# Optimization experiments

Hardware: AMD Instinct MI355X
Metric: run time of the kernel (lower is better)

Reference implementation:

```python
import jax, jax.numpy as jnp
import numpy as np
from jax import lax

S, B, I, H, T = 512, 256, 227, 100, 19


def setup_inputs() -> dict:
    key = jax.random.key(0)
    ks = jax.random.split(key, 16)
    k = 1.0 / np.sqrt(H)
    u = lambda kk, shp: jax.random.uniform(kk, shp, jnp.float32, -k, k)
    return {
        "x": jax.random.normal(ks[0], (S, B, I), jnp.float32),
        "tags": jax.random.randint(ks[1], (S, B), 0, T),
        "w_ih_f": u(ks[2], (H, I)), "w_hh_f": u(ks[3], (H, H)),
        "b_ih_f": u(ks[4], (H,)), "b_hh_f": u(ks[5], (H,)),
        "w_ih_b": u(ks[6], (H, I)), "w_hh_b": u(ks[7], (H, H)),
        "b_ih_b": u(ks[8], (H,)), "b_hh_b": u(ks[9], (H,)),
        "W_tag": u(ks[10], (T, 2 * H)), "b_tag": u(ks[11], (T,)),
        "start_t": jax.random.uniform(ks[12], (T,), jnp.float32, -0.1, 0.1),
        "end_t": jax.random.uniform(ks[13], (T,), jnp.float32, -0.1, 0.1),
        "trans": jax.random.uniform(ks[14], (T, T), jnp.float32, -0.1, 0.1),
    }


def _rnn_dir(x_proj, w_hh, b_hh):
    # x_proj: (S, B, H) precomputed input projection; tanh Elman RNN scan
    def step(h, xt):
        h = jnp.tanh(xt + h @ w_hh.T + b_hh)
        return h, h
    h0 = jnp.zeros(x_proj.shape[1:3][:1] + (w_hh.shape[0],), x_proj.dtype)
    h0 = jnp.zeros((x_proj.shape[1], w_hh.shape[0]), x_proj.dtype)
    _, hs = lax.scan(step, h0, x_proj)
    return hs  # (S, B, H)


def reference(x, tags, w_ih_f, w_hh_f, b_ih_f, b_hh_f,
              w_ih_b, w_hh_b, b_ih_b, b_hh_b,
              W_tag, b_tag, start_t, end_t, trans):
    # Bidirectional RNN
    xf = jnp.einsum('sbi,hi->sbh', x, w_ih_f) + b_ih_f
    xb = jnp.einsum('sbi,hi->sbh', x, w_ih_b) + b_ih_b
    hf = _rnn_dir(xf, w_hh_f, b_hh_f)
    hb = _rnn_dir(xb[::-1], w_hh_b, b_hh_b)[::-1]
    h = jnp.concatenate([hf, hb], axis=-1)            # (S, B, 2H)
    emissions = jnp.einsum('sbh,th->sbt', h, W_tag) + b_tag  # (S, B, T)

    # CRF numerator: score of gold tag path
    em_score = jnp.take_along_axis(emissions, tags[:, :, None], axis=2)[:, :, 0].sum(0)
    tr_score = trans[tags[:-1], tags[1:]].sum(0)
    numerator = start_t[tags[0]] + em_score + tr_score + end_t[tags[-1]]  # (B,)

    # CRF partition function: forward algorithm (log-space DP over T=19 tags)
    def fstep(score, em_t):
        # score: (B, T) -> logsumexp over previous tag
        nxt = jax.nn.logsumexp(score[:, :, None] + trans[None] + em_t[:, None, :], axis=1)
        return nxt, None
    score0 = start_t[None, :] + emissions[0]
    score, _ = lax.scan(fstep, score0, emissions[1:])
    denominator = jax.nn.logsumexp(score + end_t[None, :], axis=1)  # (B,)

    # torchcrf default reduction='sum'
    return (numerator - denominator).sum()
```

## Files before the change

kernel.cpp:

```cpp
#include <hip/hip_runtime.h>
#include <hip/hip_bf16.h>
#include <math.h>

#define S_LEN 512
#define B_SZ  256
#define I_SZ  227
#define H_SZ  100
#define T_SZ  19

__device__ __forceinline__ float tanh_fast(float x) {
    float e = __expf(2.0f * x);
    return 1.0f - 2.0f / (e + 1.0f);
}

#define LXPAD 232
__global__ __launch_bounds__(256, 2)
void k1_inproj(const float* __restrict__ x,
               const float* __restrict__ w_ih_f, const float* __restrict__ b_ih_f,
               const float* __restrict__ w_ih_b, const float* __restrict__ b_ih_b,
               float* __restrict__ xf, float* __restrict__ xb) {
    __shared__ float lx[64 * LXPAD];
    const int tid  = threadIdx.x;
    const int lane = tid & 63;
    const long m0  = (long)blockIdx.x * 64;

    {
        const int cg = tid >> 6;
        const int c0 = cg * 57;
        const int nc = (cg == 3) ? 56 : 57;
        const float* src = x + (m0 + lane) * I_SZ;
        float* dst = lx + lane * LXPAD;
        for (int i = 0; i < nc; ++i) dst[c0 + i] = src[c0 + i];
    }
    __syncthreads();

    const int jb = __builtin_amdgcn_readfirstlane(tid >> 6) * 50;
    const float* xrow = lx + lane * LXPAD;

    float acc[5][10];
    #pragma unroll
    for (int g = 0; g < 5; ++g) {
        const int j0 = jb + g * 10;
        const float* wr[10];
        #pragma unroll
        for (int u = 0; u < 10; ++u) {
            int j = j0 + u;
            if (j < 100) { wr[u] = w_ih_f + (long)j * I_SZ;         acc[g][u] = b_ih_f[j]; }
            else         { wr[u] = w_ih_b + (long)(j - 100) * I_SZ; acc[g][u] = b_ih_b[j - 100]; }
        }
        for (int k = 0; k < 224; k += 4) {
            float4 xv = *(const float4*)(xrow + k);
            #pragma unroll
            for (int u = 0; u < 10; ++u) {
                acc[g][u] = fmaf(xv.x, wr[u][k],     acc[g][u]);
                acc[g][u] = fmaf(xv.y, wr[u][k + 1], acc[g][u]);
                acc[g][u] = fmaf(xv.z, wr[u][k + 2], acc[g][u]);
                acc[g][u] = fmaf(xv.w, wr[u][k + 3], acc[g][u]);
            }
        }
        #pragma unroll
        for (int k = 224; k < 227; ++k) {
            float xv = xrow[k];
            #pragma unroll
            for (int u = 0; u < 10; ++u) acc[g][u] = fmaf(xv, wr[u][k], acc[g][u]);
        }
    }

    __syncthreads();
    #pragma unroll
    for (int g = 0; g < 5; ++g) {
        #pragma unroll
        for (int u = 0; u < 10; ++u) {
            int j = jb + g * 10 + u;
            int base = (j < 100) ? (lane * 100 + j) : (6400 + lane * 100 + (j - 100));
            lx[base] = acc[g][u];
        }
    }
    __syncthreads();

    float* dstf = xf + m0 * 100;
    float* dstb = xb + m0 * 100;
    for (int i = tid; i < 1600; i += 256) {
        ((float4*)dstf)[i] = ((const float4*)lx)[i];
        ((float4*)dstb)[i] = ((const float4*)(lx + 6400))[i];
    }
}

#define HPAD 104
__global__ __launch_bounds__(128, 1)
void k2_rnn(const float* __restrict__ w_hh_f, const float* __restrict__ b_hh_f,
            const float* __restrict__ w_hh_b, const float* __restrict__ b_hh_b,
            float* __restrict__ xf, float* __restrict__ xb) {
    __shared__ float hbuf[2][HPAD];
    const int tid = threadIdx.x;
    const int j   = tid;
    const int b   = blockIdx.x & 255;
    const int dir = blockIdx.x >> 8;

    const float* whh = dir ? w_hh_b : w_hh_f;
    const float* bhh = dir ? b_hh_b : b_hh_f;
    float* xp        = dir ? xb : xf;

    float wreg[HPAD];
    #pragma unroll
    for (int k = 0; k < HPAD; ++k) wreg[k] = 0.f;
    float bias = 0.f;
    if (j < 100) {
        bias = bhh[j];
        #pragma unroll
        for (int k = 0; k < 100; ++k) wreg[k] = whh[j * 100 + k];
    }
    if (tid < HPAD) { hbuf[0][tid] = 0.f; hbuf[1][tid] = 0.f; }
    __syncthreads();

    const int jj = (j < 100) ? j : 0;
    float cur = xp[((long)(dir ? S_LEN - 1 : 0) * B_SZ + b) * 100 + jj];

    int p = 0;
    for (int t = 0; t < S_LEN; ++t) {
        const int s  = dir ? (S_LEN - 1 - t) : t;
        const int t2 = (t + 1 < S_LEN) ? (t + 1) : t;
        const int sn = dir ? (S_LEN - 1 - t2) : t2;
        float nxt = xp[((long)sn * B_SZ + b) * 100 + jj];

        float a0 = bias, a1 = 0.f, a2 = 0.f, a3 = 0.f;
        #pragma unroll
        for (int kk = 0; kk < 26; ++kk) {
            float4 hv = *(const float4*)&hbuf[p][kk * 4];
            a0 = fmaf(wreg[4 * kk],     hv.x, a0);
            a1 = fmaf(wreg[4 * kk + 1], hv.y, a1);
            a2 = fmaf(wreg[4 * kk + 2], hv.z, a2);
            a3 = fmaf(wreg[4 * kk + 3], hv.w, a3);
        }
        float hval = tanh_fast(cur + ((a0 + a1) + (a2 + a3)));
        if (j < 100) {
            xp[((long)s * B_SZ + b) * 100 + j] = hval;
            hbuf[p ^ 1][j] = hval;
        }
        __syncthreads();
        p ^= 1;
        cur = nxt;
    }
}

__global__ __launch_bounds__(256, 4)
void k4_emis(const float* __restrict__ hf, const float* __restrict__ hb,
             const float* __restrict__ W_tag, const float* __restrict__ b_tag,
             float* __restrict__ em) {
    __shared__ float lw[T_SZ * 200];
    __shared__ float lout[64 * T_SZ];
    const int tid = threadIdx.x;
    const long m0 = (long)blockIdx.x * 64;

    for (int i = tid; i < 950; i += 256)
        ((float4*)lw)[i] = ((const float4*)W_tag)[i];
    __syncthreads();

    const int r  = tid & 63;
    const int tg = __builtin_amdgcn_readfirstlane(tid >> 6);
    const float* hfr = hf + (m0 + r) * 100;
    const float* hbr = hb + (m0 + r) * 100;

    float acc[5];
    #pragma unroll
    for (int u = 0; u < 5; ++u) {
        int t = tg + 4 * u;
        acc[u] = (t < T_SZ) ? b_tag[t] : 0.f;
    }
    for (int k = 0; k < 100; k += 4) {
        float4 hv = *(const float4*)(hfr + k);
        float4 gv = *(const float4*)(hbr + k);
        #pragma unroll
        for (int u = 0; u < 5; ++u) {
            int t = tg + 4 * u;
            if (t < T_SZ) {
                float4 wv = *(const float4*)&lw[t * 200 + k];
                float4 vv = *(const float4*)&lw[t * 200 + 100 + k];
                acc[u] = fmaf(hv.x, wv.x, acc[u]); acc[u] = fmaf(hv.y, wv.y, acc[u]);
                acc[u] = fmaf(hv.z, wv.z, acc[u]); acc[u] = fmaf(hv.w, wv.w, acc[u]);
                acc[u] = fmaf(gv.x, vv.x, acc[u]); acc[u] = fmaf(gv.y, vv.y, acc[u]);
                acc[u] = fmaf(gv.z, vv.z, acc[u]); acc[u] = fmaf(gv.w, vv.w, acc[u]);
            }
        }
    }
    #pragma unroll
    for (int u = 0; u < 5; ++u) {
        int t = tg + 4 * u;
        if (t < T_SZ) lout[r * T_SZ + t] = acc[u];
    }
    __syncthreads();

    float* dst = em + m0 * T_SZ;
    for (int i = tid; i < 304; i += 256)
        ((float4*)dst)[i] = ((const float4*)lout)[i];
}

__global__ __launch_bounds__(64)
void k5_numer(const int* __restrict__ tags, const float* __restrict__ em,
              const float* __restrict__ trans, const float* __restrict__ start_t,
              const float* __restrict__ end_t, float* __restrict__ num) {
    const int b   = blockIdx.x;
    const int tid = threadIdx.x;
    float acc = 0.f;
    #pragma unroll
    for (int i = 0; i < 8; ++i) {
        int s  = tid + i * 64;
        int ts = tags[(long)s * B_SZ + b];
        acc += em[((long)s * B_SZ + b) * T_SZ + ts];
        if (s < S_LEN - 1) {
            int tn = tags[(long)(s + 1) * B_SZ + b];
            acc += trans[ts * T_SZ + tn];
        }
    }
    if (tid == 0)  acc += start_t[tags[b]];
    if (tid == 63) acc += end_t[tags[(long)(S_LEN - 1) * B_SZ + b]];
    #pragma unroll
    for (int off = 32; off; off >>= 1) acc += __shfl_down(acc, off, 64);
    if (tid == 0) num[b] = acc;
}

__global__ __launch_bounds__(64)
void k6_crf(const float* __restrict__ em, const float* __restrict__ trans,
            const float* __restrict__ start_t, const float* __restrict__ end_t,
            const float* __restrict__ num, float* __restrict__ out) {
    __shared__ float sbuf[2][3][20];
    const int tid = threadIdx.x;
    const int bl  = tid / T_SZ;
    const int j   = tid - bl * T_SZ;
    const int b   = blockIdx.x * 3 + bl;
    const bool act = (tid < 57) && (b < B_SZ);

    float texp[T_SZ];
    float score = 0.f, em_cur = 0.f;
    if (act) {
        #pragma unroll
        for (int i = 0; i < T_SZ; ++i) texp[i] = __expf(trans[i * T_SZ + j]);
        score  = start_t[j] + em[(long)b * T_SZ + j];
        em_cur = em[((long)1 * B_SZ + b) * T_SZ + j];
    }

    int buf = 0;
    for (int s = 1; s < S_LEN; ++s) {
        float em_nxt = 0.f;
        if (act) {
            int sn = (s + 1 < S_LEN) ? (s + 1) : s;
            em_nxt = em[((long)sn * B_SZ + b) * T_SZ + j];
            sbuf[buf][bl][j] = score;
        }
        __syncthreads();
        if (act) {
            float4 v0 = *(const float4*)&sbuf[buf][bl][0];
            float4 v1 = *(const float4*)&sbuf[buf][bl][4];
            float4 v2 = *(const float4*)&sbuf[buf][bl][8];
            float4 v3 = *(const float4*)&sbuf[buf][bl][12];
            float4 v4 = *(const float4*)&sbuf[buf][bl][16];
            float sc[T_SZ] = {v0.x,v0.y,v0.z,v0.w, v1.x,v1.y,v1.z,v1.w,
                              v2.x,v2.y,v2.z,v2.w, v3.x,v3.y,v3.z,v3.w,
                              v4.x,v4.y,v4.z};
            float m = sc[0];
            #pragma unroll
            for (int i = 0; i < 9; ++i) m = fmaxf(fmaxf(m, sc[2*i+1]), sc[2*i+2]);
            float sum = 0.f;
            #pragma unroll
            for (int i = 0; i < T_SZ; ++i) sum = fmaf(__expf(sc[i] - m), texp[i], sum);
            score = m + __logf(sum) + em_cur;
        }
        em_cur = em_nxt;
        buf ^= 1;
    }

    if (act) sbuf[0][bl][j] = score + end_t[j];
    __syncthreads();
    if (act && j == 0) {
        float m = -1e30f;
        #pragma unroll
        for (int i = 0; i < T_SZ; ++i) m = fmaxf(m, sbuf[0][bl][i]);
        float sum = 0.f;
        #pragma unroll
        for (int i = 0; i < T_SZ; ++i) sum += __expf(sbuf[0][bl][i] - m);
        atomicAdd(out, num[b] - (m + __logf(sum)));
    }
}

extern "C" void kernel_launch(void* const* d_in, const int* in_sizes, int n_in,
                              void* d_out, int out_size, void* d_ws, size_t ws_size,
                              hipStream_t stream) {
    const float* x       = (const float*)d_in[0];
    const int*   tags    = (const int*)  d_in[1];
    const float* w_ih_f  = (const float*)d_in[2];
    const float* w_hh_f  = (const float*)d_in[3];
    const float* b_ih_f  = (const float*)d_in[4];
    const float* b_hh_f  = (const float*)d_in[5];
    const float* w_ih_b  = (const float*)d_in[6];
    const float* w_hh_b  = (const float*)d_in[7];
    const float* b_ih_b  = (const float*)d_in[8];
    const float* b_hh_b  = (const float*)d_in[9];
    const float* W_tag   = (const float*)d_in[10];
    const float* b_tag   = (const float*)d_in[11];
    const float* start_t = (const float*)d_in[12];
    const float* end_t   = (const float*)d_in[13];
    const float* trans   = (const float*)d_in[14];

    float* ws = (float*)d_ws;
    float* xf  = ws;
    float* xb  = xf + 13107200;
    float* em  = xb + 13107200;
    float* num = em + 2490368;

    k1_inproj<<<2048, 256, 0, stream>>>(x, w_ih_f, b_ih_f, w_ih_b, b_ih_b, xf, xb);
    k2_rnn   <<<512, 128, 0, stream>>>(w_hh_f, b_hh_f, w_hh_b, b_hh_b, xf, xb);
    k4_emis  <<<2048, 256, 0, stream>>>(xf, xb, W_tag, b_tag, em);
    k5_numer <<<256, 64, 0, stream>>>(tags, em, trans, start_t, end_t, num);
    hipMemsetAsync(d_out, 0, sizeof(float), stream);
    k6_crf   <<<86, 64, 0, stream>>>(em, trans, start_t, end_t, num, (float*)d_out);
}
```

Before: 1.528 ms.

## Stage input-projection weights in LDS and coalesce x tile loads

The input-projection kernel now copies the 64-row x tile with coalesced float4 global loads, then remaps it into padded LDS rows. Each wave stages 25 weight rows at a time in its own LDS region and reads them as float4 from LDS, where before it read scalar weights from global memory. It keeps 50 accumulators per thread and uses dynamic shared memory of about 150 KB, with launch bounds lowered to one block per CU. The aim is to remove uncoalesced global weight reads and strided x loads, at the cost of lower occupancy, more LDS traffic and extra barriers.

```diff
diff --git a/kernel.cpp b/kernel.cpp
--- a/kernel.cpp
+++ b/kernel.cpp
@@ -13,68 +13,86 @@
     return 1.0f - 2.0f / (e + 1.0f);
 }
 
-#define LXPAD 232
-__global__ __launch_bounds__(256, 2)
+#define XTP 228
+#define K1_LDS ((64 + 4 * 25) * XTP * 4)
+
+__global__ __launch_bounds__(256, 1)
 void k1_inproj(const float* __restrict__ x,
                const float* __restrict__ w_ih_f, const float* __restrict__ b_ih_f,
                const float* __restrict__ w_ih_b, const float* __restrict__ b_ih_b,
                float* __restrict__ xf, float* __restrict__ xb) {
-    __shared__ float lx[64 * LXPAD];
+    extern __shared__ float smem[];
+    float* lx = smem;
     const int tid  = threadIdx.x;
     const int lane = tid & 63;
+    const int wv   = __builtin_amdgcn_readfirstlane(tid >> 6);
+    float* lwv = smem + 64 * XTP + wv * 25 * XTP;
     const long m0  = (long)blockIdx.x * 64;
 
     {
-        const int cg = tid >> 6;
-        const int c0 = cg * 57;
-        const int nc = (cg == 3) ? 56 : 57;
-        const float* src = x + (m0 + lane) * I_SZ;
-        float* dst = lx + lane * LXPAD;
-        for (int i = 0; i < nc; ++i) dst[c0 + i] = src[c0 + i];
-    }
-    __syncthreads();
-
-    const int jb = __builtin_amdgcn_readfirstlane(tid >> 6) * 50;
-    const float* xrow = lx + lane * LXPAD;
-
-    float acc[5][10];
-    #pragma unroll
-    for (int g = 0; g < 5; ++g) {
-        const int j0 = jb + g * 10;
-        const float* wr[10];
-        #pragma unroll
-        for (int u = 0; u < 10; ++u) {
-            int j = j0 + u;
-            if (j < 100) { wr[u] = w_ih_f + (long)j * I_SZ;         acc[g][u] = b_ih_f[j]; }
-            else         { wr[u] = w_ih_b + (long)(j - 100) * I_SZ; acc[g][u] = b_ih_b[j - 100]; }
-        }
+        const float* xsrc = x + m0 * I_SZ;
+        for (int i = tid; i < 3632; i += 256) {
+            float4 v = ((const float4*)xsrc)[i];
+            int f = i * 4;
+            #pragma unroll
+            for (int e = 0; e < 4; ++e) {
+                int fe = f + e;
+                int r  = fe / I_SZ;
+                int c  = fe - r * I_SZ;
+                float val = (e == 0) ? v.x : (e == 1) ? v.y : (e == 2) ? v.z : v.w;
+                lx[r * XTP + c] = val;
+            }
+        }
+    }
+    __syncthreads();
+
+    const int jb = wv * 50;
+    const float* xrow = lx + lane * XTP;
+
+    float acc[50];
+    #pragma unroll
+    for (int u = 0; u < 50; ++u) {
+        int j = jb + u;
+        acc[u] = (j < 100) ? b_ih_f[j] : b_ih_b[j - 100];
+    }
+
+    #pragma unroll
+    for (int c = 0; c < 2; ++c) {
+        const int j0 = jb + c * 25;
+        const float* ws = (j0 < 100) ? (w_ih_f + (long)j0 * I_SZ)
+                                     : (w_ih_b + (long)(j0 - 100) * I_SZ);
+        #pragma unroll
+        for (int u = 0; u < 25; ++u)
+            for (int i = lane; i < I_SZ; i += 64)
+                lwv[u * XTP + i] = ws[u * I_SZ + i];
+        __syncthreads();
+
         for (int k = 0; k < 224; k += 4) {
             float4 xv = *(const float4*)(xrow + k);
             #pragma unroll
-            for (int u = 0; u < 10; ++u) {
-                acc[g][u] = fmaf(xv.x, wr[u][k],     acc[g][u]);
-                acc[g][u] = fmaf(xv.y, wr[u][k + 1], acc[g][u]);
-                acc[g][u] = fmaf(xv.z, wr[u][k + 2], acc[g][u]);
-                acc[g][u] = fmaf(xv.w, wr[u][k + 3], acc[g][u]);
+            for (int u = 0; u < 25; ++u) {
+                float4 wvv = *(const float4*)(lwv + u * XTP + k);
+                acc[c * 25 + u] = fmaf(xv.x, wvv.x, acc[c * 25 + u]);
+                acc[c * 25 + u] = fmaf(xv.y, wvv.y, acc[c * 25 + u]);
+                acc[c * 25 + u] = fmaf(xv.z, wvv.z, acc[c * 25 + u]);
+                acc[c * 25 + u] = fmaf(xv.w, wvv.w, acc[c * 25 + u]);
             }
         }
         #pragma unroll
         for (int k = 224; k < 227; ++k) {
             float xv = xrow[k];
             #pragma unroll
-            for (int u = 0; u < 10; ++u) acc[g][u] = fmaf(xv, wr[u][k], acc[g][u]);
-        }
-    }
-
-    __syncthreads();
-    #pragma unroll
-    for (int g = 0; g < 5; ++g) {
-        #pragma unroll
-        for (int u = 0; u < 10; ++u) {
-            int j = jb + g * 10 + u;
-            int base = (j < 100) ? (lane * 100 + j) : (6400 + lane * 100 + (j - 100));
-            lx[base] = acc[g][u];
-        }
+            for (int u = 0; u < 25; ++u)
+                acc[c * 25 + u] = fmaf(xv, lwv[u * XTP + k], acc[c * 25 + u]);
+        }
+        __syncthreads();
+    }
+
+    #pragma unroll
+    for (int u = 0; u < 50; ++u) {
+        int j = jb + u;
+        int base = (j < 100) ? (lane * 100 + j) : (6400 + lane * 100 + (j - 100));
+        lx[base] = acc[u];
     }
     __syncthreads();
 
@@ -307,7 +325,10 @@
     float* em  = xb + 13107200;
     float* num = em + 2490368;
 
-    k1_inproj<<<2048, 256, 0, stream>>>(x, w_ih_f, b_ih_f, w_ih_b, b_ih_b, xf, xb);
+    hipFuncSetAttribute((const void*)k1_inproj,
+                        hipFuncAttributeMaxDynamicSharedMemorySize, K1_LDS);
+
+    k1_inproj<<<2048, 256, K1_LDS, stream>>>(x, w_ih_f, b_ih_f, w_ih_b, b_ih_b, xf, xb);
     k2_rnn   <<<512, 128, 0, stream>>>(w_hh_f, b_hh_f, w_hh_b, b_hh_b, xf, xb);
     k4_emis  <<<2048, 256, 0, stream>>>(xf, xb, W_tag, b_tag, em);
     k5_numer <<<256, 64, 0, stream>>>(tags, em, trans, start_t, end_t, num);
```

Result: slower. 1.828 ms (+19.7%).
